# Optimization experiments

Hardware: AMD Instinct MI355X
Metric: run time of the kernel (lower is better)

Reference implementation:

```python
import jax, jax.numpy as jnp
import numpy as np
from jax import lax

B, N, C = 256, 128, 256
GRID_SIZE = 0.05
# eta/phi are sampled in [0, 2), so (v - min)/0.05 < 40 -> grid index <= 39.
# Using a static 40x40 grid is mathematically identical to the dynamic
# H = max+1, W = max+1 of the original: extra rows/cols are zero, which
# matches the 'same' zero padding the depthwise conv would see anyway,
# and gathered positions are unchanged.
HMAX, WMAX = 40, 40
KH = KW = 3


def setup_inputs() -> dict:
    key = jax.random.key(0)
    ks = jax.random.split(key, 9)
    x = jax.random.normal(ks[0], (B, N, C), jnp.float32)
    eta = jax.random.uniform(ks[1], (B, N), jnp.float32, 0.0, 2.0)
    phi = jax.random.uniform(ks[2], (B, N), jnp.float32, 0.0, 2.0)
    # depthwise conv kernel, HWIO with I = in_channels/groups = 1
    conv_kernel = jax.random.normal(ks[3], (KH, KW, 1, C), jnp.float32) * 0.1
    conv_bias = jax.random.normal(ks[4], (C,), jnp.float32) * 0.01
    dense_w = jax.random.normal(ks[5], (C, C), jnp.float32) * (1.0 / np.sqrt(C))
    dense_b = jax.random.normal(ks[6], (C,), jnp.float32) * 0.01
    gamma = jnp.ones((C,), jnp.float32)
    beta = jnp.zeros((C,), jnp.float32)
    return {
        "x": x, "eta": eta, "phi": phi,
        "conv_kernel": conv_kernel, "conv_bias": conv_bias,
        "dense_w": dense_w, "dense_b": dense_b,
        "gamma": gamma, "beta": beta,
    }


def reference(x, eta, phi, conv_kernel, conv_bias, dense_w, dense_b, gamma, beta):
    Bq, Nq, Cq = x.shape
    # quantize particle positions to grid bins (per-batch min shift)
    ge = ((eta - eta.min(axis=1, keepdims=True)) / GRID_SIZE).astype(jnp.int32)  # [B,N]
    gp = ((phi - phi.min(axis=1, keepdims=True)) / GRID_SIZE).astype(jnp.int32)  # [B,N]
    b_idx = jnp.arange(Bq)[:, None]  # broadcasts against [B,N]

    # scatter-add particle features into dense (eta,phi) grid
    grid = jnp.zeros((Bq, HMAX, WMAX, Cq), x.dtype).at[b_idx, ge, gp].add(x)

    # depthwise 3x3 conv, 'same' zero padding, per-channel bias
    grid = lax.conv_general_dilated(
        grid, conv_kernel, window_strides=(1, 1), padding="SAME",
        dimension_numbers=("NHWC", "HWIO", "NHWC"), feature_group_count=Cq,
    ) + conv_bias

    # gather back to particles
    out = grid[b_idx, ge, gp]  # [B, N, C]

    # pointwise dense
    out = jnp.einsum("bnc,cd->bnd", out, dense_w) + dense_b

    # layer norm (eps=1e-6, biased variance, channel affine)
    mean = out.mean(axis=-1, keepdims=True)
    var = jnp.mean(jnp.square(out - mean), axis=-1, keepdims=True)
    out = (out - mean) * lax.rsqrt(var + 1e-6) * gamma + beta

    return x + out
```

## Files before the change

### kernel.cpp

```cpp
#include <hip/hip_runtime.h>

typedef __attribute__((ext_vector_type(8))) short bf16x8;
typedef __attribute__((ext_vector_type(4))) float f32x4;

#define Bq 256
#define Nq 128
#define Cq 256
#define TP 16
#define NBLK (Nq / TP)

__device__ __forceinline__ unsigned short f2bf(float f) {
    unsigned int u = __float_as_uint(f);
    u += 0x7fffu + ((u >> 16) & 1u);
    return (unsigned short)(u >> 16);
}

struct ushort4_t { unsigned short x, y, z, w; };

__device__ __forceinline__ void fma4(float4& a, const float4& k, const float4& x) {
    a.x = fmaf(k.x, x.x, a.x);
    a.y = fmaf(k.y, x.y, a.y);
    a.z = fmaf(k.z, x.z, a.z);
    a.w = fmaf(k.w, x.w, a.w);
}

__global__ __launch_bounds__(256) void wpack_kernel(const float* __restrict__ dw,
                                                    unsigned short* __restrict__ wp) {
    int tid = blockIdx.x * 256 + threadIdx.x;
    int j    = tid & 7;
    int lane = (tid >> 3) & 63;
    int nt   = (tid >> 9) & 15;
    int kt   = tid >> 13;
    int k = kt * 32 + (lane >> 4) * 8 + j;
    int n = nt * 16 + (lane & 15);
    wp[tid] = f2bf(dw[k * Cq + n]);
}

__global__ __launch_bounds__(256, 4) void fused_kernel(
    const float* __restrict__ x, const float* __restrict__ eta, const float* __restrict__ phi,
    const float* __restrict__ ck, const float* __restrict__ cb,
    const unsigned short* __restrict__ wp, const float* __restrict__ db,
    const float* __restrict__ gamma, const float* __restrict__ beta,
    float* __restrict__ out) {
    const int b  = blockIdx.x >> 3;
    const int p0 = (blockIdx.x & (NBLK - 1)) * TP;
    const int t  = threadIdx.x;
    const int lane = t & 63, wave = t >> 6;

    __shared__ int   s_cnt[TP];
    __shared__ unsigned short s_list[TP][132];
    __shared__ unsigned short s_A[8 * 64 * 8] __attribute__((aligned(16)));
    __shared__ float s_sum[TP][4], s_sq[TP][4];

    const int pp = t >> 4, cg = t & 15;

    float e0 = eta[b * Nq + lane], e1 = eta[b * Nq + 64 + lane];
    float q0 = phi[b * Nq + lane], q1 = phi[b * Nq + 64 + lane];
    float emin = fminf(e0, e1), pmin = fminf(q0, q1);
#pragma unroll
    for (int off = 32; off > 0; off >>= 1) {
        emin = fminf(emin, __shfl_xor(emin, off));
        pmin = fminf(pmin, __shfl_xor(pmin, off));
    }
    int ge0 = (int)((e0 - emin) / 0.05f), ge1 = (int)((e1 - emin) / 0.05f);
    int gp0 = (int)((q0 - pmin) / 0.05f), gp1 = (int)((q1 - pmin) / 0.05f);

    if ((lane >> 4) == 0) s_cnt[4 * wave + (lane & 3)] = 0;
    __threadfence_block();

    {
        int P = p0 + pp;
        int pa = (P & 63) << 2;
        int tel = __builtin_amdgcn_ds_bpermute(pa, ge0);
        int teh = __builtin_amdgcn_ds_bpermute(pa, ge1);
        int tpl = __builtin_amdgcn_ds_bpermute(pa, gp0);
        int tph = __builtin_amdgcn_ds_bpermute(pa, gp1);
        int th = (P < 64) ? tel : teh;
        int tw = (P < 64) ? tpl : tph;
#pragma unroll
        for (int i = 0; i < 8; ++i) {
            int m = cg * 8 + i;
            int ma = (m & 63) << 2;
            int mel = __builtin_amdgcn_ds_bpermute(ma, ge0);
            int meh = __builtin_amdgcn_ds_bpermute(ma, ge1);
            int mpl = __builtin_amdgcn_ds_bpermute(ma, gp0);
            int mph = __builtin_amdgcn_ds_bpermute(ma, gp1);
            int me = (m < 64) ? mel : meh;
            int mp = (m < 64) ? mpl : mph;
            int dh = me - th, dv = mp - tw;
            if (dh >= -1 && dh <= 1 && dv >= -1 && dv <= 1) {
                int k = (dh + 1) * 3 + (dv + 1);
                int pos = atomicAdd(&s_cnt[pp], 1);
                s_list[pp][pos] = (unsigned short)(m | (k << 7));
            }
        }
    }
    __threadfence_block();

    {
        const float4* x4  = (const float4*)x + (size_t)b * (Nq * Cq / 4) + cg;
        const float4* ck4 = (const float4*)ck + cg;
        const float4* cb4 = (const float4*)cb + cg;
        float4 a0 = cb4[0], a1 = cb4[16], a2 = cb4[32], a3 = cb4[48];

        const int cnt = s_cnt[pp];
        const unsigned short* lst = s_list[pp];
        int i = 0;
        for (; i + 2 <= cnt; i += 2) {
            int e0_ = lst[i], e1_ = lst[i + 1];
            const float4* xp0 = x4  + ((e0_ & 127) << 6);
            const float4* kp0 = ck4 + ((e0_ >> 7)  << 6);
            const float4* xp1 = x4  + ((e1_ & 127) << 6);
            const float4* kp1 = ck4 + ((e1_ >> 7)  << 6);
            float4 X00 = xp0[0], X01 = xp0[16], X02 = xp0[32], X03 = xp0[48];
            float4 X10 = xp1[0], X11 = xp1[16], X12 = xp1[32], X13 = xp1[48];
            float4 K00 = kp0[0], K01 = kp0[16], K02 = kp0[32], K03 = kp0[48];
            float4 K10 = kp1[0], K11 = kp1[16], K12 = kp1[32], K13 = kp1[48];
            fma4(a0, K00, X00); fma4(a1, K01, X01);
            fma4(a2, K02, X02); fma4(a3, K03, X03);
            fma4(a0, K10, X10); fma4(a1, K11, X11);
            fma4(a2, K12, X12); fma4(a3, K13, X13);
        }
        if (i < cnt) {
            int e0_ = lst[i];
            const float4* xp0 = x4  + ((e0_ & 127) << 6);
            const float4* kp0 = ck4 + ((e0_ >> 7)  << 6);
            float4 X00 = xp0[0], X01 = xp0[16], X02 = xp0[32], X03 = xp0[48];
            float4 K00 = kp0[0], K01 = kp0[16], K02 = kp0[32], K03 = kp0[48];
            fma4(a0, K00, X00); fma4(a1, K01, X01);
            fma4(a2, K02, X02); fma4(a3, K03, X03);
        }

        const int g = (cg >> 1) & 3;
        const int lidx = ((pp + 2 * g) & 15) | (g << 4);
        const int off = (cg & 1) * 4;
        float4 aj[4] = {a0, a1, a2, a3};
#pragma unroll
        for (int j = 0; j < 4; ++j) {
            int kt = j * 2 + (cg >> 3);
            ushort4_t v;
            v.x = f2bf(aj[j].x); v.y = f2bf(aj[j].y);
            v.z = f2bf(aj[j].z); v.w = f2bf(aj[j].w);
            *(ushort4_t*)&s_A[(kt * 64 + lidx) * 8 + off] = v;
        }
    }
    __syncthreads();

    f32x4 acc[4];
#pragma unroll
    for (int ntl = 0; ntl < 4; ++ntl) acc[ntl] = (f32x4){0.f, 0.f, 0.f, 0.f};

    const int g2 = lane >> 4, m2 = lane & 15;
    const int alidx = ((m2 + 2 * g2) & 15) | (g2 << 4);
#pragma unroll
    for (int kt2 = 0; kt2 < 8; ++kt2) {
        bf16x8 af = *reinterpret_cast<const bf16x8*>(&s_A[(kt2 * 64 + alidx) * 8]);
#pragma unroll
        for (int ntl = 0; ntl < 4; ++ntl) {
            int nt = wave * 4 + ntl;
            bf16x8 bfr = *reinterpret_cast<const bf16x8*>(&wp[((kt2 * 16 + nt) * 64 + lane) * 8]);
            acc[ntl] = __builtin_amdgcn_mfma_f32_16x16x32_bf16(af, bfr, acc[ntl], 0, 0, 0);
        }
    }

    float dbv[4], gv[4], bv[4];
#pragma unroll
    for (int ntl = 0; ntl < 4; ++ntl) {
        int col = (wave * 4 + ntl) * 16 + m2;
        dbv[ntl] = db[col]; gv[ntl] = gamma[col]; bv[ntl] = beta[col];
    }
#pragma unroll
    for (int r = 0; r < 4; ++r) {
        float a = 0.f, q = 0.f;
#pragma unroll
        for (int ntl = 0; ntl < 4; ++ntl) {
            float y = acc[ntl][r] + dbv[ntl];
            a += y; q += y * y;
        }
#pragma unroll
        for (int off = 8; off >= 1; off >>= 1) {
            a += __shfl_xor(a, off);
            q += __shfl_xor(q, off);
        }
        if (m2 == 0) {
            int row = g2 * 4 + r;
            s_sum[row][wave] = a;
            s_sq[row][wave]  = q;
        }
    }
    __syncthreads();

#pragma unroll
    for (int r = 0; r < 4; ++r) {
        int row = g2 * 4 + r;
        float s = s_sum[row][0] + s_sum[row][1] + s_sum[row][2] + s_sum[row][3];
        float q = s_sq[row][0] + s_sq[row][1] + s_sq[row][2] + s_sq[row][3];
        float mean = s * (1.0f / Cq);
        float var  = q * (1.0f / Cq) - mean * mean;
        float inv  = rsqrtf(var + 1e-6f);
        int gbase = (b * Nq + p0 + row) * Cq + wave * 64 + m2;
#pragma unroll
        for (int ntl = 0; ntl < 4; ++ntl) {
            float y = acc[ntl][r] + dbv[ntl];
            int idx = gbase + ntl * 16;
            out[idx] = x[idx] + (y - mean) * inv * gv[ntl] + bv[ntl];
        }
    }
}

extern "C" void kernel_launch(void* const* d_in, const int* in_sizes, int n_in,
                              void* d_out, int out_size, void* d_ws, size_t ws_size,
                              hipStream_t stream) {
    const float* x     = (const float*)d_in[0];
    const float* eta   = (const float*)d_in[1];
    const float* phi   = (const float*)d_in[2];
    const float* ck    = (const float*)d_in[3];
    const float* cb    = (const float*)d_in[4];
    const float* dw    = (const float*)d_in[5];
    const float* db    = (const float*)d_in[6];
    const float* gamma = (const float*)d_in[7];
    const float* beta  = (const float*)d_in[8];
    float* out = (float*)d_out;

    unsigned short* wpk = (unsigned short*)d_ws;

    wpack_kernel<<<Cq, 256, 0, stream>>>(dw, wpk);
    fused_kernel<<<Bq * NBLK, 256, 0, stream>>>(x, eta, phi, ck, cb, wpk, db,
                                                gamma, beta, out);
}
```

Measured before the change: 117.2 us.

## Split fused kernel into conv and GEMM kernels via global staging

Splits the fused gather-conv and GEMM+layernorm kernel into two launches, writing the bf16 MFMA A-fragments to a workspace buffer in global memory. It also packs eta/phi grid indices into one int to halve cross-lane permutes, and prefetches the residual x before the MFMA loop. The intent is lower per-kernel register and LDS pressure and better overlap. In exchange it adds a global write and read of the intermediate tile plus an extra kernel launch.

```diff
diff --git a/kernel.cpp b/kernel.cpp
--- a/kernel.cpp
+++ b/kernel.cpp
@@ -36,21 +36,18 @@
     wp[tid] = f2bf(dw[k * Cq + n]);
 }
 
-__global__ __launch_bounds__(256, 4) void fused_kernel(
+__global__ __launch_bounds__(256, 4) void conv_kernel(
     const float* __restrict__ x, const float* __restrict__ eta, const float* __restrict__ phi,
     const float* __restrict__ ck, const float* __restrict__ cb,
-    const unsigned short* __restrict__ wp, const float* __restrict__ db,
-    const float* __restrict__ gamma, const float* __restrict__ beta,
-    float* __restrict__ out) {
-    const int b  = blockIdx.x >> 3;
-    const int p0 = (blockIdx.x & (NBLK - 1)) * TP;
+    unsigned short* __restrict__ afr) {
+    const int blk = blockIdx.x;
+    const int b  = blk >> 3;
+    const int p0 = (blk & (NBLK - 1)) * TP;
     const int t  = threadIdx.x;
     const int lane = t & 63, wave = t >> 6;
 
-    __shared__ int   s_cnt[TP];
+    __shared__ int s_cnt[TP];
     __shared__ unsigned short s_list[TP][132];
-    __shared__ unsigned short s_A[8 * 64 * 8] __attribute__((aligned(16)));
-    __shared__ float s_sum[TP][4], s_sq[TP][4];
 
     const int pp = t >> 4, cg = t & 15;
 
@@ -62,8 +59,8 @@
         emin = fminf(emin, __shfl_xor(emin, off));
         pmin = fminf(pmin, __shfl_xor(pmin, off));
     }
-    int ge0 = (int)((e0 - emin) / 0.05f), ge1 = (int)((e1 - emin) / 0.05f);
-    int gp0 = (int)((q0 - pmin) / 0.05f), gp1 = (int)((q1 - pmin) / 0.05f);
+    int pk0 = ((int)((e0 - emin) / 0.05f) << 8) | (int)((q0 - pmin) / 0.05f);
+    int pk1 = ((int)((e1 - emin) / 0.05f) << 8) | (int)((q1 - pmin) / 0.05f);
 
     if ((lane >> 4) == 0) s_cnt[4 * wave + (lane & 3)] = 0;
     __threadfence_block();
@@ -71,23 +68,18 @@
     {
         int P = p0 + pp;
         int pa = (P & 63) << 2;
-        int tel = __builtin_amdgcn_ds_bpermute(pa, ge0);
-        int teh = __builtin_amdgcn_ds_bpermute(pa, ge1);
-        int tpl = __builtin_amdgcn_ds_bpermute(pa, gp0);
-        int tph = __builtin_amdgcn_ds_bpermute(pa, gp1);
-        int th = (P < 64) ? tel : teh;
-        int tw = (P < 64) ? tpl : tph;
+        int t0 = __builtin_amdgcn_ds_bpermute(pa, pk0);
+        int t1 = __builtin_amdgcn_ds_bpermute(pa, pk1);
+        int tp = (P < 64) ? t0 : t1;
+        int th = tp >> 8, tw = tp & 255;
 #pragma unroll
         for (int i = 0; i < 8; ++i) {
             int m = cg * 8 + i;
             int ma = (m & 63) << 2;
-            int mel = __builtin_amdgcn_ds_bpermute(ma, ge0);
-            int meh = __builtin_amdgcn_ds_bpermute(ma, ge1);
-            int mpl = __builtin_amdgcn_ds_bpermute(ma, gp0);
-            int mph = __builtin_amdgcn_ds_bpermute(ma, gp1);
-            int me = (m < 64) ? mel : meh;
-            int mp = (m < 64) ? mpl : mph;
-            int dh = me - th, dv = mp - tw;
+            int c0 = __builtin_amdgcn_ds_bpermute(ma, pk0);
+            int c1 = __builtin_amdgcn_ds_bpermute(ma, pk1);
+            int cp = (cg < 8) ? c0 : c1;
+            int dh = (cp >> 8) - th, dv = (cp & 255) - tw;
             if (dh >= -1 && dh <= 1 && dv >= -1 && dv <= 1) {
                 int k = (dh + 1) * 3 + (dv + 1);
                 int pos = atomicAdd(&s_cnt[pp], 1);
@@ -97,64 +89,85 @@
     }
     __threadfence_block();
 
-    {
-        const float4* x4  = (const float4*)x + (size_t)b * (Nq * Cq / 4) + cg;
-        const float4* ck4 = (const float4*)ck + cg;
-        const float4* cb4 = (const float4*)cb + cg;
-        float4 a0 = cb4[0], a1 = cb4[16], a2 = cb4[32], a3 = cb4[48];
-
-        const int cnt = s_cnt[pp];
-        const unsigned short* lst = s_list[pp];
-        int i = 0;
-        for (; i + 2 <= cnt; i += 2) {
-            int e0_ = lst[i], e1_ = lst[i + 1];
-            const float4* xp0 = x4  + ((e0_ & 127) << 6);
-            const float4* kp0 = ck4 + ((e0_ >> 7)  << 6);
-            const float4* xp1 = x4  + ((e1_ & 127) << 6);
-            const float4* kp1 = ck4 + ((e1_ >> 7)  << 6);
-            float4 X00 = xp0[0], X01 = xp0[16], X02 = xp0[32], X03 = xp0[48];
-            float4 X10 = xp1[0], X11 = xp1[16], X12 = xp1[32], X13 = xp1[48];
-            float4 K00 = kp0[0], K01 = kp0[16], K02 = kp0[32], K03 = kp0[48];
-            float4 K10 = kp1[0], K11 = kp1[16], K12 = kp1[32], K13 = kp1[48];
-            fma4(a0, K00, X00); fma4(a1, K01, X01);
-            fma4(a2, K02, X02); fma4(a3, K03, X03);
-            fma4(a0, K10, X10); fma4(a1, K11, X11);
-            fma4(a2, K12, X12); fma4(a3, K13, X13);
-        }
-        if (i < cnt) {
-            int e0_ = lst[i];
-            const float4* xp0 = x4  + ((e0_ & 127) << 6);
-            const float4* kp0 = ck4 + ((e0_ >> 7)  << 6);
-            float4 X00 = xp0[0], X01 = xp0[16], X02 = xp0[32], X03 = xp0[48];
-            float4 K00 = kp0[0], K01 = kp0[16], K02 = kp0[32], K03 = kp0[48];
-            fma4(a0, K00, X00); fma4(a1, K01, X01);
-            fma4(a2, K02, X02); fma4(a3, K03, X03);
-        }
-
-        const int g = (cg >> 1) & 3;
-        const int lidx = ((pp + 2 * g) & 15) | (g << 4);
-        const int off = (cg & 1) * 4;
-        float4 aj[4] = {a0, a1, a2, a3};
-#pragma unroll
-        for (int j = 0; j < 4; ++j) {
-            int kt = j * 2 + (cg >> 3);
-            ushort4_t v;
-            v.x = f2bf(aj[j].x); v.y = f2bf(aj[j].y);
-            v.z = f2bf(aj[j].z); v.w = f2bf(aj[j].w);
-            *(ushort4_t*)&s_A[(kt * 64 + lidx) * 8 + off] = v;
-        }
-    }
-    __syncthreads();
-
-    f32x4 acc[4];
-#pragma unroll
-    for (int ntl = 0; ntl < 4; ++ntl) acc[ntl] = (f32x4){0.f, 0.f, 0.f, 0.f};
+    const float4* x4  = (const float4*)x + (size_t)b * (Nq * Cq / 4) + cg;
+    const float4* ck4 = (const float4*)ck + cg;
+    const float4* cb4 = (const float4*)cb + cg;
+    float4 a0 = cb4[0], a1 = cb4[16], a2 = cb4[32], a3 = cb4[48];
+
+    const int cnt = s_cnt[pp];
+    const unsigned short* lst = s_list[pp];
+    int i = 0;
+    for (; i + 2 <= cnt; i += 2) {
+        int e0_ = lst[i], e1_ = lst[i + 1];
+        const float4* xp0 = x4  + ((e0_ & 127) << 6);
+        const float4* kp0 = ck4 + ((e0_ >> 7)  << 6);
+        const float4* xp1 = x4  + ((e1_ & 127) << 6);
+        const float4* kp1 = ck4 + ((e1_ >> 7)  << 6);
+        float4 X00 = xp0[0], X01 = xp0[16], X02 = xp0[32], X03 = xp0[48];
+        float4 X10 = xp1[0], X11 = xp1[16], X12 = xp1[32], X13 = xp1[48];
+        float4 K00 = kp0[0], K01 = kp0[16], K02 = kp0[32], K03 = kp0[48];
+        float4 K10 = kp1[0], K11 = kp1[16], K12 = kp1[32], K13 = kp1[48];
+        fma4(a0, K00, X00); fma4(a1, K01, X01);
+        fma4(a2, K02, X02); fma4(a3, K03, X03);
+        fma4(a0, K10, X10); fma4(a1, K11, X11);
+        fma4(a2, K12, X12); fma4(a3, K13, X13);
+    }
+    if (i < cnt) {
+        int e0_ = lst[i];
+        const float4* xp0 = x4  + ((e0_ & 127) << 6);
+        const float4* kp0 = ck4 + ((e0_ >> 7)  << 6);
+        float4 X00 = xp0[0], X01 = xp0[16], X02 = xp0[32], X03 = xp0[48];
+        float4 K00 = kp0[0], K01 = kp0[16], K02 = kp0[32], K03 = kp0[48];
+        fma4(a0, K00, X00); fma4(a1, K01, X01);
+        fma4(a2, K02, X02); fma4(a3, K03, X03);
+    }
+
+    unsigned short* ab = afr + (size_t)blk * 4096;
+    const int g = (cg >> 1) & 3;
+    const int lidx = ((pp + 2 * g) & 15) | (g << 4);
+    const int off = (cg & 1) * 4;
+    float4 aj[4] = {a0, a1, a2, a3};
+#pragma unroll
+    for (int j = 0; j < 4; ++j) {
+        int kt = j * 2 + (cg >> 3);
+        ushort4_t v;
+        v.x = f2bf(aj[j].x); v.y = f2bf(aj[j].y);
+        v.z = f2bf(aj[j].z); v.w = f2bf(aj[j].w);
+        *(ushort4_t*)&ab[(kt * 64 + lidx) * 8 + off] = v;
+    }
+}
+
+__global__ __launch_bounds__(256, 4) void gemm_kernel(
+    const float* __restrict__ x, const unsigned short* __restrict__ afr,
+    const unsigned short* __restrict__ wp, const float* __restrict__ db,
+    const float* __restrict__ gamma, const float* __restrict__ beta,
+    float* __restrict__ out) {
+    const int blk = blockIdx.x;
+    const int b  = blk >> 3;
+    const int p0 = (blk & (NBLK - 1)) * TP;
+    const int lane = threadIdx.x & 63, wave = threadIdx.x >> 6;
+
+    __shared__ float s_sum[TP][4], s_sq[TP][4];
 
     const int g2 = lane >> 4, m2 = lane & 15;
     const int alidx = ((m2 + 2 * g2) & 15) | (g2 << 4);
+    const unsigned short* ab = afr + (size_t)blk * 4096;
+
+    float xr[4][4];
+    const int gbase0 = (b * Nq + p0 + g2 * 4) * Cq + wave * 64 + m2;
+#pragma unroll
+    for (int r = 0; r < 4; ++r)
+#pragma unroll
+        for (int ntl = 0; ntl < 4; ++ntl)
+            xr[r][ntl] = x[gbase0 + r * Cq + ntl * 16];
+
+    f32x4 acc[4];
+#pragma unroll
+    for (int ntl = 0; ntl < 4; ++ntl) acc[ntl] = (f32x4){0.f, 0.f, 0.f, 0.f};
+
 #pragma unroll
     for (int kt2 = 0; kt2 < 8; ++kt2) {
-        bf16x8 af = *reinterpret_cast<const bf16x8*>(&s_A[(kt2 * 64 + alidx) * 8]);
+        bf16x8 af = *reinterpret_cast<const bf16x8*>(&ab[(kt2 * 64 + alidx) * 8]);
 #pragma unroll
         for (int ntl = 0; ntl < 4; ++ntl) {
             int nt = wave * 4 + ntl;
@@ -202,8 +215,7 @@
 #pragma unroll
         for (int ntl = 0; ntl < 4; ++ntl) {
             float y = acc[ntl][r] + dbv[ntl];
-            int idx = gbase + ntl * 16;
-            out[idx] = x[idx] + (y - mean) * inv * gv[ntl] + bv[ntl];
+            out[gbase + ntl * 16] = xr[r][ntl] + (y - mean) * inv * gv[ntl] + bv[ntl];
         }
     }
 }
@@ -223,8 +235,9 @@
     float* out = (float*)d_out;
 
     unsigned short* wpk = (unsigned short*)d_ws;
+    unsigned short* afr = wpk + 65536;
 
     wpack_kernel<<<Cq, 256, 0, stream>>>(dw, wpk);
-    fused_kernel<<<Bq * NBLK, 256, 0, stream>>>(x, eta, phi, ck, cb, wpk, db,
-                                                gamma, beta, out);
-}
+    conv_kernel<<<Bq * NBLK, 256, 0, stream>>>(x, eta, phi, ck, cb, afr);
+    gemm_kernel<<<Bq * NBLK, 256, 0, stream>>>(x, afr, wpk, db, gamma, beta, out);
+}
```

After: 126.1 us. 1.08x slower.

## Process 32 particles per block with two MFMA row tiles and LDS conv weights

Applied to the files above, without the earlier changes.

Doubles the particles per block from 16 to 32. Each thread now builds neighbour lists for two particles and computes two conv results. The GEMM issues two MFMA row tiles per weight fragment, so each loaded weight fragment is reused twice. The conv kernel is staged into LDS, and eta/phi bins are packed into one int to halve the bpermute count. The cost is fewer blocks (1024), more LDS per block and more registers, which may lower occupancy.

```diff
diff --git a/kernel.cpp b/kernel.cpp
--- a/kernel.cpp
+++ b/kernel.cpp
@@ -6,7 +6,7 @@
 #define Bq 256
 #define Nq 128
 #define Cq 256
-#define TP 16
+#define TP 32
 #define NBLK (Nq / TP)
 
 __device__ __forceinline__ unsigned short f2bf(float f) {
@@ -42,14 +42,15 @@
     const unsigned short* __restrict__ wp, const float* __restrict__ db,
     const float* __restrict__ gamma, const float* __restrict__ beta,
     float* __restrict__ out) {
-    const int b  = blockIdx.x >> 3;
+    const int b  = blockIdx.x >> 2;
     const int p0 = (blockIdx.x & (NBLK - 1)) * TP;
     const int t  = threadIdx.x;
     const int lane = t & 63, wave = t >> 6;
 
+    __shared__ float s_ck[9 * Cq];
     __shared__ int   s_cnt[TP];
-    __shared__ unsigned short s_list[TP][132];
-    __shared__ unsigned short s_A[8 * 64 * 8] __attribute__((aligned(16)));
+    __shared__ unsigned short s_list[TP][130];
+    __shared__ unsigned short s_A[2 * 8 * 64 * 8] __attribute__((aligned(16)));
     __shared__ float s_sum[TP][4], s_sq[TP][4];
 
     const int pp = t >> 4, cg = t & 15;
@@ -62,104 +63,119 @@
         emin = fminf(emin, __shfl_xor(emin, off));
         pmin = fminf(pmin, __shfl_xor(pmin, off));
     }
-    int ge0 = (int)((e0 - emin) / 0.05f), ge1 = (int)((e1 - emin) / 0.05f);
-    int gp0 = (int)((q0 - pmin) / 0.05f), gp1 = (int)((q1 - pmin) / 0.05f);
-
-    if ((lane >> 4) == 0) s_cnt[4 * wave + (lane & 3)] = 0;
-    __threadfence_block();
+    int pk0 = ((int)((e0 - emin) / 0.05f) << 8) | (int)((q0 - pmin) / 0.05f);
+    int pk1 = ((int)((e1 - emin) / 0.05f) << 8) | (int)((q1 - pmin) / 0.05f);
+
+    for (int i = t; i < 9 * Cq; i += 256) s_ck[i] = ck[i];
+    if (t < TP) s_cnt[t] = 0;
+    __syncthreads();
 
     {
-        int P = p0 + pp;
-        int pa = (P & 63) << 2;
-        int tel = __builtin_amdgcn_ds_bpermute(pa, ge0);
-        int teh = __builtin_amdgcn_ds_bpermute(pa, ge1);
-        int tpl = __builtin_amdgcn_ds_bpermute(pa, gp0);
-        int tph = __builtin_amdgcn_ds_bpermute(pa, gp1);
-        int th = (P < 64) ? tel : teh;
-        int tw = (P < 64) ? tpl : tph;
+        int PA = p0 + pp, PB = PA + 16;
+        int a0_ = __builtin_amdgcn_ds_bpermute((PA & 63) << 2, pk0);
+        int a1_ = __builtin_amdgcn_ds_bpermute((PA & 63) << 2, pk1);
+        int b0_ = __builtin_amdgcn_ds_bpermute((PB & 63) << 2, pk0);
+        int b1_ = __builtin_amdgcn_ds_bpermute((PB & 63) << 2, pk1);
+        int tpA = (PA < 64) ? a0_ : a1_;
+        int tpB = (PB < 64) ? b0_ : b1_;
+        int thA = tpA >> 8, twA = tpA & 255;
+        int thB = tpB >> 8, twB = tpB & 255;
 #pragma unroll
         for (int i = 0; i < 8; ++i) {
             int m = cg * 8 + i;
             int ma = (m & 63) << 2;
-            int mel = __builtin_amdgcn_ds_bpermute(ma, ge0);
-            int meh = __builtin_amdgcn_ds_bpermute(ma, ge1);
-            int mpl = __builtin_amdgcn_ds_bpermute(ma, gp0);
-            int mph = __builtin_amdgcn_ds_bpermute(ma, gp1);
-            int me = (m < 64) ? mel : meh;
-            int mp = (m < 64) ? mpl : mph;
-            int dh = me - th, dv = mp - tw;
-            if (dh >= -1 && dh <= 1 && dv >= -1 && dv <= 1) {
-                int k = (dh + 1) * 3 + (dv + 1);
+            int c0 = __builtin_amdgcn_ds_bpermute(ma, pk0);
+            int c1 = __builtin_amdgcn_ds_bpermute(ma, pk1);
+            int cp = (cg < 8) ? c0 : c1;
+            int mh = cp >> 8, mw = cp & 255;
+            int dhA = mh - thA, dvA = mw - twA;
+            if (dhA >= -1 && dhA <= 1 && dvA >= -1 && dvA <= 1) {
+                int k = (dhA + 1) * 3 + (dvA + 1);
                 int pos = atomicAdd(&s_cnt[pp], 1);
                 s_list[pp][pos] = (unsigned short)(m | (k << 7));
             }
+            int dhB = mh - thB, dvB = mw - twB;
+            if (dhB >= -1 && dhB <= 1 && dvB >= -1 && dvB <= 1) {
+                int k = (dhB + 1) * 3 + (dvB + 1);
+                int pos = atomicAdd(&s_cnt[pp + 16], 1);
+                s_list[pp + 16][pos] = (unsigned short)(m | (k << 7));
+            }
         }
     }
     __threadfence_block();
 
     {
         const float4* x4  = (const float4*)x + (size_t)b * (Nq * Cq / 4) + cg;
-        const float4* ck4 = (const float4*)ck + cg;
+        const float4* ck4 = (const float4*)s_ck + cg;
         const float4* cb4 = (const float4*)cb + cg;
-        float4 a0 = cb4[0], a1 = cb4[16], a2 = cb4[32], a3 = cb4[48];
-
-        const int cnt = s_cnt[pp];
-        const unsigned short* lst = s_list[pp];
-        int i = 0;
-        for (; i + 2 <= cnt; i += 2) {
-            int e0_ = lst[i], e1_ = lst[i + 1];
-            const float4* xp0 = x4  + ((e0_ & 127) << 6);
-            const float4* kp0 = ck4 + ((e0_ >> 7)  << 6);
-            const float4* xp1 = x4  + ((e1_ & 127) << 6);
-            const float4* kp1 = ck4 + ((e1_ >> 7)  << 6);
-            float4 X00 = xp0[0], X01 = xp0[16], X02 = xp0[32], X03 = xp0[48];
-            float4 X10 = xp1[0], X11 = xp1[16], X12 = xp1[32], X13 = xp1[48];
-            float4 K00 = kp0[0], K01 = kp0[16], K02 = kp0[32], K03 = kp0[48];
-            float4 K10 = kp1[0], K11 = kp1[16], K12 = kp1[32], K13 = kp1[48];
-            fma4(a0, K00, X00); fma4(a1, K01, X01);
-            fma4(a2, K02, X02); fma4(a3, K03, X03);
-            fma4(a0, K10, X10); fma4(a1, K11, X11);
-            fma4(a2, K12, X12); fma4(a3, K13, X13);
-        }
-        if (i < cnt) {
-            int e0_ = lst[i];
-            const float4* xp0 = x4  + ((e0_ & 127) << 6);
-            const float4* kp0 = ck4 + ((e0_ >> 7)  << 6);
-            float4 X00 = xp0[0], X01 = xp0[16], X02 = xp0[32], X03 = xp0[48];
-            float4 K00 = kp0[0], K01 = kp0[16], K02 = kp0[32], K03 = kp0[48];
-            fma4(a0, K00, X00); fma4(a1, K01, X01);
-            fma4(a2, K02, X02); fma4(a3, K03, X03);
-        }
-
         const int g = (cg >> 1) & 3;
-        const int lidx = ((pp + 2 * g) & 15) | (g << 4);
         const int off = (cg & 1) * 4;
-        float4 aj[4] = {a0, a1, a2, a3};
-#pragma unroll
-        for (int j = 0; j < 4; ++j) {
-            int kt = j * 2 + (cg >> 3);
-            ushort4_t v;
-            v.x = f2bf(aj[j].x); v.y = f2bf(aj[j].y);
-            v.z = f2bf(aj[j].z); v.w = f2bf(aj[j].w);
-            *(ushort4_t*)&s_A[(kt * 64 + lidx) * 8 + off] = v;
+
+#pragma unroll
+        for (int half = 0; half < 2; ++half) {
+            const int lp = pp + half * 16;
+            float4 a0 = cb4[0], a1 = cb4[16], a2 = cb4[32], a3 = cb4[48];
+            const int cnt = s_cnt[lp];
+            const unsigned short* lst = s_list[lp];
+            int i = 0;
+            for (; i + 2 <= cnt; i += 2) {
+                int e0_ = lst[i], e1_ = lst[i + 1];
+                const float4* xp0 = x4  + ((e0_ & 127) << 6);
+                const float4* kp0 = ck4 + ((e0_ >> 7)  << 6);
+                const float4* xp1 = x4  + ((e1_ & 127) << 6);
+                const float4* kp1 = ck4 + ((e1_ >> 7)  << 6);
+                float4 X00 = xp0[0], X01 = xp0[16], X02 = xp0[32], X03 = xp0[48];
+                float4 X10 = xp1[0], X11 = xp1[16], X12 = xp1[32], X13 = xp1[48];
+                float4 K00 = kp0[0], K01 = kp0[16], K02 = kp0[32], K03 = kp0[48];
+                float4 K10 = kp1[0], K11 = kp1[16], K12 = kp1[32], K13 = kp1[48];
+                fma4(a0, K00, X00); fma4(a1, K01, X01);
+                fma4(a2, K02, X02); fma4(a3, K03, X03);
+                fma4(a0, K10, X10); fma4(a1, K11, X11);
+                fma4(a2, K12, X12); fma4(a3, K13, X13);
+            }
+            if (i < cnt) {
+                int e0_ = lst[i];
+                const float4* xp0 = x4  + ((e0_ & 127) << 6);
+                const float4* kp0 = ck4 + ((e0_ >> 7)  << 6);
+                float4 X00 = xp0[0], X01 = xp0[16], X02 = xp0[32], X03 = xp0[48];
+                float4 K00 = kp0[0], K01 = kp0[16], K02 = kp0[32], K03 = kp0[48];
+                fma4(a0, K00, X00); fma4(a1, K01, X01);
+                fma4(a2, K02, X02); fma4(a3, K03, X03);
+            }
+
+            const int pl = pp;
+            const int lidx = ((pl + 2 * g) & 15) | (g << 4);
+            float4 aj[4] = {a0, a1, a2, a3};
+#pragma unroll
+            for (int j = 0; j < 4; ++j) {
+                int kt = j * 2 + (cg >> 3);
+                ushort4_t v;
+                v.x = f2bf(aj[j].x); v.y = f2bf(aj[j].y);
+                v.z = f2bf(aj[j].z); v.w = f2bf(aj[j].w);
+                *(ushort4_t*)&s_A[((half * 8 + kt) * 64 + lidx) * 8 + off] = v;
+            }
         }
     }
     __syncthreads();
 
-    f32x4 acc[4];
-#pragma unroll
-    for (int ntl = 0; ntl < 4; ++ntl) acc[ntl] = (f32x4){0.f, 0.f, 0.f, 0.f};
+    f32x4 acc[2][4];
+#pragma unroll
+    for (int mt = 0; mt < 2; ++mt)
+#pragma unroll
+        for (int ntl = 0; ntl < 4; ++ntl) acc[mt][ntl] = (f32x4){0.f, 0.f, 0.f, 0.f};
 
     const int g2 = lane >> 4, m2 = lane & 15;
     const int alidx = ((m2 + 2 * g2) & 15) | (g2 << 4);
 #pragma unroll
     for (int kt2 = 0; kt2 < 8; ++kt2) {
-        bf16x8 af = *reinterpret_cast<const bf16x8*>(&s_A[(kt2 * 64 + alidx) * 8]);
+        bf16x8 af0 = *reinterpret_cast<const bf16x8*>(&s_A[((0 * 8 + kt2) * 64 + alidx) * 8]);
+        bf16x8 af1 = *reinterpret_cast<const bf16x8*>(&s_A[((1 * 8 + kt2) * 64 + alidx) * 8]);
 #pragma unroll
         for (int ntl = 0; ntl < 4; ++ntl) {
             int nt = wave * 4 + ntl;
             bf16x8 bfr = *reinterpret_cast<const bf16x8*>(&wp[((kt2 * 16 + nt) * 64 + lane) * 8]);
-            acc[ntl] = __builtin_amdgcn_mfma_f32_16x16x32_bf16(af, bfr, acc[ntl], 0, 0, 0);
+            acc[0][ntl] = __builtin_amdgcn_mfma_f32_16x16x32_bf16(af0, bfr, acc[0][ntl], 0, 0, 0);
+            acc[1][ntl] = __builtin_amdgcn_mfma_f32_16x16x32_bf16(af1, bfr, acc[1][ntl], 0, 0, 0);
         }
     }
 
@@ -170,11 +186,13 @@
         dbv[ntl] = db[col]; gv[ntl] = gamma[col]; bv[ntl] = beta[col];
     }
 #pragma unroll
+    for (int mt = 0; mt < 2; ++mt)
+#pragma unroll
     for (int r = 0; r < 4; ++r) {
         float a = 0.f, q = 0.f;
 #pragma unroll
         for (int ntl = 0; ntl < 4; ++ntl) {
-            float y = acc[ntl][r] + dbv[ntl];
+            float y = acc[mt][ntl][r] + dbv[ntl];
             a += y; q += y * y;
         }
 #pragma unroll
@@ -183,7 +201,7 @@
             q += __shfl_xor(q, off);
         }
         if (m2 == 0) {
-            int row = g2 * 4 + r;
+            int row = mt * 16 + g2 * 4 + r;
             s_sum[row][wave] = a;
             s_sq[row][wave]  = q;
         }
@@ -191,8 +209,10 @@
     __syncthreads();
 
 #pragma unroll
+    for (int mt = 0; mt < 2; ++mt)
+#pragma unroll
     for (int r = 0; r < 4; ++r) {
-        int row = g2 * 4 + r;
+        int row = mt * 16 + g2 * 4 + r;
         float s = s_sum[row][0] + s_sum[row][1] + s_sum[row][2] + s_sum[row][3];
         float q = s_sq[row][0] + s_sq[row][1] + s_sq[row][2] + s_sq[row][3];
         float mean = s * (1.0f / Cq);
@@ -201,7 +221,7 @@
         int gbase = (b * Nq + p0 + row) * Cq + wave * 64 + m2;
 #pragma unroll
         for (int ntl = 0; ntl < 4; ++ntl) {
-            float y = acc[ntl][r] + dbv[ntl];
+            float y = acc[mt][ntl][r] + dbv[ntl];
             int idx = gbase + ntl * 16;
             out[idx] = x[idx] + (y - mean) * inv * gv[ntl] + bv[ntl];
         }
```

Result: no change. 116.4 us (-0.7%).
